# Kernel optimization log

Hardware: AMD Instinct MI355X
Metric: run time of the kernel (lower is better)

Reference implementation:

```python
import jax, jax.numpy as jnp
import numpy as np

N = 307
T = 6000
ED = 96
DIM_FC = 95712  # 16 * 5982
EPS_BN = 1e-5
TEMP = 0.5


def _conv1d(x, w, b):
    # x: [B, Cin, L], w: [Cout, Cin, K]
    y = jax.lax.conv_general_dilated(x, w, (1,), 'VALID',
                                     dimension_numbers=('NCH', 'OIH', 'NCH'))
    return y + b[None, :, None]


def _bn_nch(x, g, b):
    # BatchNorm1d on [B, C, L] in train mode (batch stats, biased var)
    m = jnp.mean(x, axis=(0, 2), keepdims=True)
    v = jnp.var(x, axis=(0, 2), keepdims=True)
    return g[None, :, None] * (x - m) * jax.lax.rsqrt(v + EPS_BN) + b[None, :, None]


def setup_inputs() -> dict:
    key = jax.random.key(0)
    ks = jax.random.split(key, 10)
    return {
        'long_term_history': jax.random.normal(ks[0], (32, 864, N), jnp.float32),
        'node_feats': jax.random.normal(ks[1], (T, N), jnp.float32),
        'conv1_w': jax.random.normal(ks[2], (8, 1, 10), jnp.float32) * 0.3,
        'conv1_b': jnp.zeros((8,), jnp.float32),
        'conv2_w': jax.random.normal(ks[3], (16, 8, 10), jnp.float32) * 0.1,
        'conv2_b': jnp.zeros((16,), jnp.float32),
        'bn1_g': jnp.ones((8,), jnp.float32),
        'bn1_b': jnp.zeros((8,), jnp.float32),
        'bn2_g': jnp.ones((16,), jnp.float32),
        'bn2_b': jnp.zeros((16,), jnp.float32),
        'bn3_g': jnp.ones((ED,), jnp.float32),
        'bn3_b': jnp.zeros((ED,), jnp.float32),
        'fc_w': jax.random.normal(ks[4], (DIM_FC, ED), jnp.float32) * 0.003,
        'fc_b': jnp.zeros((ED,), jnp.float32),
        'fc_out_w': jax.random.normal(ks[5], (2 * ED, ED), jnp.float32) * 0.07,
        'fc_out_b': jnp.zeros((ED,), jnp.float32),
        'fc_cat_w': jax.random.normal(ks[6], (ED, 2), jnp.float32) * 0.1,
        'fc_cat_b': jnp.zeros((2,), jnp.float32),
        'uniform': jax.random.uniform(ks[7], (N, N, 2), jnp.float32),
    }


def reference(long_term_history, node_feats, conv1_w, conv1_b, conv2_w, conv2_b,
              bn1_g, bn1_b, bn2_g, bn2_b, bn3_g, bn3_b, fc_w, fc_b,
              fc_out_w, fc_out_b, fc_cat_w, fc_cat_b, uniform):
    num_nodes = long_term_history.shape[2]
    # ---- node encoder (conv -> bn -> conv -> bn -> fc -> bn) ----
    x = node_feats.T[:, None, :]                              # [N, 1, T]
    x = _bn_nch(jax.nn.relu(_conv1d(x, conv1_w, conv1_b)), bn1_g, bn1_b)
    x = _bn_nch(jax.nn.relu(_conv1d(x, conv2_w, conv2_b)), bn2_g, bn2_b)
    x = x.reshape(num_nodes, -1)                              # [N, 95712]
    x = jax.nn.relu(x @ fc_w + fc_b)                          # [N, 96]
    m = jnp.mean(x, axis=0, keepdims=True)
    v = jnp.var(x, axis=0, keepdims=True)
    node_feat = bn3_g * (x - m) * jax.lax.rsqrt(v + EPS_BN) + bn3_b
    # ---- edge features: cat([sender, receiver]) @ W == s@Ws + r@Wr ----
    # edge e = i*N + j: sender = node_feat[j], receiver = node_feat[i]
    d = fc_out_w.shape[0] // 2
    s_proj = node_feat @ fc_out_w[:d]                         # [N, 96]
    r_proj = node_feat @ fc_out_w[d:]                         # [N, 96]
    edge_feat = jax.nn.relu(r_proj[:, None, :] + s_proj[None, :, :] + fc_out_b)  # [N, N, 96]
    logits = edge_feat @ fc_cat_w + fc_cat_b                  # [N, N, 2]
    # ---- hard gumbel-softmax ----
    gumbel = -jnp.log(-jnp.log(uniform + 1e-20) + 1e-20)
    y_soft = jax.nn.softmax((logits + gumbel) / TEMP, axis=-1)
    y_hard = jax.nn.one_hot(jnp.argmax(y_soft, axis=-1), 2, dtype=y_soft.dtype)
    y = jax.lax.stop_gradient(y_hard - y_soft) + y_soft
    adj = y[..., 0] * (1.0 - jnp.eye(num_nodes, dtype=y.dtype))  # zero diagonal
    return adj
```

## Files before the change

### kernel.cpp

```cpp
#include <hip/hip_runtime.h>
#include <hip/hip_fp16.h>

#define N_NODES 307
#define T_LEN   6000
#define L1      5991
#define L2      5982
#define ED      96
#define FDIM    95712
#define NCH2    16
#define LCPC    16
#define CHL     374
#define K5CH    (NCH2 * LCPC)
#define K3L     32
#define K3ZP    43
#define K3LB    187
#define K3NB    20
#define K3BLKS  (K3LB * K3NB)
#define K4ABLK  40
#define CSUB    8
#define CSROWS  47

static const size_t WS_P1 = 256;
static const size_t WS_P2 = 8192;
static const size_t WS_P4D = 127872;
static const size_t WS_NF = 155648;
static const size_t WS_SP = 188416;
static const size_t WS_RP = 221184;
static const size_t WS_A2 = 262144;
static const size_t WS_FP = 262144 + 30627840ull;
static const size_t WS_BP = 30889984ull + 7864320ull;
static const size_t WS_CS2 = 38754304ull + 9188352ull;

typedef _Float16 half8 __attribute__((ext_vector_type(8)));
typedef float f32x4 __attribute__((ext_vector_type(4)));

union U4H8 { uint4 u; half8 h; };

__device__ __forceinline__ unsigned int pack2h(float x) {
  __half h = __float2half(x);
  float r = (x - __half2float(h)) * 2048.0f;
  __half l = __float2half(r);
  return (unsigned int)__half_as_ushort(h) | ((unsigned int)__half_as_ushort(l) << 16);
}

__device__ __forceinline__ void split2h(float x, unsigned short& ho, unsigned short& lo) {
  __half h = __float2half(x);
  float r = (x - __half2float(h)) * 2048.0f;
  __half l = __float2half(r);
  ho = __half_as_ushort(h);
  lo = __half_as_ushort(l);
}

__device__ __forceinline__ void unpackU4(const uint4& a0, const uint4& a1,
                                         U4H8& hi, U4H8& lo) {
  hi.u = make_uint4((a0.x & 0xFFFFu) | (a0.y << 16), (a0.z & 0xFFFFu) | (a0.w << 16),
                    (a1.x & 0xFFFFu) | (a1.y << 16), (a1.z & 0xFFFFu) | (a1.w << 16));
  lo.u = make_uint4((a0.x >> 16) | (a0.y & 0xFFFF0000u), (a0.z >> 16) | (a0.w & 0xFFFF0000u),
                    (a1.x >> 16) | (a1.y & 0xFFFF0000u), (a1.z >> 16) | (a1.w & 0xFFFF0000u));
}

__device__ __forceinline__ int swz16(int e, int k) {
  return e * 192 + (k ^ ((e & 7) << 3));
}

__global__ __launch_bounds__(320) void dgl_k1_conv1_stats(
    const float* __restrict__ nfeat, const float* __restrict__ w1,
    const float* __restrict__ b1, float* __restrict__ ws) {
  __shared__ float sw1[80], sb1[8];
  __shared__ float sred[5][16];
  int tid = threadIdx.x;
  if (tid < 80) sw1[tid] = w1[tid];
  if (tid < 8)  sb1[tid] = b1[tid];
  __syncthreads();
  int l0 = blockIdx.x * 16;
  int n = tid;
  bool nv = n < N_NODES;
  float xx[26];
#pragma unroll
  for (int j = 0; j < 26; ++j) {
    int t = l0 + j;
    xx[j] = (nv && t < T_LEN) ? nfeat[(size_t)t * N_NODES + n] : 0.f;
  }
  float s[8], q[8];
#pragma unroll
  for (int c = 0; c < 8; ++c) { s[c] = 0.f; q[c] = 0.f; }
#pragma unroll
  for (int dl = 0; dl < 16; ++dl) {
    int l = l0 + dl;
    if (nv && l < L1) {
#pragma unroll
      for (int c = 0; c < 8; ++c) {
        float r = sb1[c];
#pragma unroll
        for (int k = 0; k < 10; ++k) r = fmaf(xx[dl + k], sw1[c * 10 + k], r);
        float z = fmaxf(r, 0.f);
        s[c] += z; q[c] += z * z;
      }
    }
  }
  int wv = tid >> 6, ln = tid & 63;
#pragma unroll
  for (int c = 0; c < 8; ++c) {
    float vs = s[c], vq = q[c];
    for (int o = 32; o; o >>= 1) { vs += __shfl_down(vs, o, 64); vq += __shfl_down(vq, o, 64); }
    if (ln == 0) { sred[wv][c] = vs; sred[wv][8 + c] = vq; }
  }
  __syncthreads();
  if (tid < 16) {
    float t = 0.f;
    for (int w = 0; w < 5; ++w) t += sred[w][tid];
    ws[WS_P1 + (size_t)blockIdx.x * 16 + tid] = t;
  }
}

__global__ void dgl_k2_fin1(const float* __restrict__ g1, const float* __restrict__ b1,
                            float* __restrict__ ws) {
  __shared__ double sd[16];
  int tid = threadIdx.x;
  if (tid < 16) {
    double a = 0.0;
    for (int j = 0; j < 375; ++j) a += (double)ws[WS_P1 + (size_t)j * 16 + tid];
    sd[tid] = a;
  }
  __syncthreads();
  if (tid < 8) {
    double cnt = (double)N_NODES * (double)L1;
    double m = sd[tid] / cnt;
    double v = sd[tid + 8] / cnt - m * m;
    double inv = 1.0 / sqrt(v + 1e-5);
    ws[tid]     = (float)((double)g1[tid] * inv);
    ws[8 + tid] = (float)((double)b1[tid] - (double)g1[tid] * inv * m);
  }
}

__global__ __launch_bounds__(256, 4) void dgl_k3_conv2(
    const float* __restrict__ nfeat, const float* __restrict__ w1, const float* __restrict__ b1,
    const float* __restrict__ w2, const float* __restrict__ b2, float* __restrict__ ws) {
  __shared__ __align__(16) unsigned short z1h[K3ZP * 128];
  __shared__ __align__(16) unsigned short z1l[K3ZP * 128];
  __shared__ __align__(16) unsigned short w2h[16 * 96], w2l[16 * 96];
  __shared__ float sw1[80], sb1[8], ss1[8], st1[8], sb2v[16];
  __shared__ float wps[4][4][4], wpq[4][4][4];
  int tid = threadIdx.x;
  int l0b = blockIdx.x * K3L, n0 = blockIdx.y * 16;
  unsigned int* a2u = (unsigned int*)(ws + WS_A2);

  if (tid < 80) sw1[tid] = w1[tid];
  if (tid < 8)  { sb1[tid] = b1[tid]; ss1[tid] = ws[tid]; st1[tid] = ws[8 + tid]; }
  if (tid < 16) sb2v[tid] = b2[tid];
  for (int i = tid; i < 16 * 96; i += 256) {
    int c2 = i / 96, kk = i % 96;
    float v = (kk < 80) ? w2[c2 * 80 + (kk & 7) * 10 + (kk >> 3)] : 0.f;
    unsigned short ho, lo;
    split2h(v, ho, lo);
    w2h[i] = ho; w2l[i] = lo;
  }
  __syncthreads();
  {
    int n = tid & 15, cin = (tid >> 4) & 7, hf = tid >> 7;
    int lp0 = hf ? 22 : 0;
    int cnt = hf ? 21 : 22;
    int nld = hf ? 30 : 31;
    int nglob0 = n0 + n;
    bool nv = nglob0 < N_NODES;
    float xx[31];
#pragma unroll
    for (int j = 0; j < 31; ++j) {
      int t = l0b + lp0 + j;
      xx[j] = (j < nld && nv && t < T_LEN) ? nfeat[(size_t)t * N_NODES + nglob0] : 0.f;
    }
    float wr[10];
#pragma unroll
    for (int k = 0; k < 10; ++k) wr[k] = sw1[cin * 10 + k];
    float bb = sb1[cin], sc = ss1[cin], sh = st1[cin];
#pragma unroll
    for (int o = 0; o < 22; ++o) {
      if (o < cnt) {
        float r = bb;
#pragma unroll
        for (int k = 0; k < 10; ++k) r = fmaf(xx[o + k], wr[k], r);
        float z = fmaf(sc, fmaxf(r, 0.f), sh);
        unsigned short ho, lo;
        split2h(z, ho, lo);
        int lp = lp0 + o;
        int idx = lp * 128 + ((n ^ (lp & 15)) << 3) + cin;
        z1h[idx] = ho; z1l[idx] = lo;
      }
    }
  }
  __syncthreads();

  int wv = tid >> 6, lane = tid & 63;
  int m = lane & 15, g = lane >> 4;
  U4H8 Ahi[3], Alo[3];
#pragma unroll
  for (int s = 0; s < 3; ++s) {
    Ahi[s].u = *(const uint4*)(&w2h[m * 96 + 32 * s + 8 * g]);
    Alo[s].u = *(const uint4*)(&w2l[m * 96 + 32 * s + 8 * g]);
  }
  float sv[4] = {0.f, 0.f, 0.f, 0.f}, qv[4] = {0.f, 0.f, 0.f, 0.f};
  int nglob = n0 + m;
  bool nok = nglob < N_NODES;
#pragma unroll 1
  for (int li = 0; li < 8; ++li) {
    int ll = 8 * wv + li;
    int lg = l0b + ll;
    f32x4 ac1 = (f32x4){0.f, 0.f, 0.f, 0.f};
    f32x4 ac2 = (f32x4){0.f, 0.f, 0.f, 0.f};
#pragma unroll
    for (int s = 0; s < 3; ++s) {
      int lp = ll + 4 * s + g;
      int bpidx = lp * 128 + ((m ^ (lp & 15)) << 3);
      U4H8 Bhi, Blo;
      Bhi.u = *(const uint4*)(&z1h[bpidx]);
      Blo.u = *(const uint4*)(&z1l[bpidx]);
      ac1 = __builtin_amdgcn_mfma_f32_16x16x32_f16(Ahi[s].h, Bhi.h, ac1, 0, 0, 0);
      ac2 = __builtin_amdgcn_mfma_f32_16x16x32_f16(Ahi[s].h, Blo.h, ac2, 0, 0, 0);
      ac2 = __builtin_amdgcn_mfma_f32_16x16x32_f16(Alo[s].h, Bhi.h, ac2, 0, 0, 0);
    }
    if (lg < L2) {
#pragma unroll
      for (int r = 0; r < 4; ++r) {
        float v = ac1[r] + ac2[r] * (1.0f / 2048.0f) + sb2v[4 * g + r];
        v = fmaxf(v, 0.f);
        if (!nok) v = 0.f;
        sv[r] += v; qv[r] += v * v;
        a2u[((size_t)(4 * g + r) * L2 + lg) * 320 + nglob] = pack2h(v);
      }
    }
  }
#pragma unroll
  for (int r = 0; r < 4; ++r) {
    for (int o = 1; o < 16; o <<= 1) {
      sv[r] += __shfl_xor(sv[r], o, 64);
      qv[r] += __shfl_xor(qv[r], o, 64);
    }
  }
  if (m == 0) {
#pragma unroll
    for (int r = 0; r < 4; ++r) { wps[wv][g][r] = sv[r]; wpq[wv][g][r] = qv[r]; }
  }
  __syncthreads();
  if (tid < 32) {
    int c2 = tid & 15; bool isq = tid >= 16;
    int gg = c2 >> 2, rr = c2 & 3;
    float t = 0.f;
    for (int w = 0; w < 4; ++w) t += isq ? wpq[w][gg][rr] : wps[w][gg][rr];
    ws[WS_P2 + ((size_t)blockIdx.y * gridDim.x + blockIdx.x) * 32 + tid] = t;
  }
}

__global__ __launch_bounds__(512) void dgl_k4a(float* __restrict__ ws) {
  __shared__ double red[16][32];
  int tid = threadIdx.x, blk = blockIdx.x;
  int v = tid & 31, p = tid >> 5;
  double a = 0.0;
#pragma unroll
  for (int k = 0; k < 6; ++k) {
    int idx = p + 16 * k;
    int j = blk * 94 + idx;
    if (idx < 94 && j < K3BLKS) a += (double)ws[WS_P2 + (size_t)j * 32 + v];
  }
  red[p][v] = a;
  __syncthreads();
  if (p == 0) {
    double s = 0.0;
    for (int q = 0; q < 16; ++q) s += red[q][v];
    ((double*)(ws + WS_P4D))[(size_t)blk * 32 + v] = s;
  }
}

__global__ void dgl_k4b2_fin(const float* __restrict__ g2, const float* __restrict__ b2,
                             float* __restrict__ ws) {
  __shared__ double sd[32];
  int tid = threadIdx.x;
  if (tid < 32) {
    const double* pd = (const double*)(ws + WS_P4D);
    double s = 0.0;
    for (int b = 0; b < K4ABLK; ++b) s += pd[(size_t)b * 32 + tid];
    sd[tid] = s;
  }
  __syncthreads();
  if (tid < 16) {
    double cnt = (double)N_NODES * (double)L2;
    double m = sd[tid] / cnt;
    double var = sd[tid + 16] / cnt - m * m;
    double inv = 1.0 / sqrt(var + 1e-5);
    ws[16 + tid] = (float)((double)g2[tid] * inv);
    ws[32 + tid] = (float)((double)b2[tid] - (double)g2[tid] * inv * m);
  }
}

__global__ __launch_bounds__(256) void dgl_k4b_colsum(const float* __restrict__ fcw,
                                                      float* __restrict__ ws) {
  __shared__ float red[10][96];
  int b = blockIdx.x;
  int ch = b >> 3, sub = b & 7;
  int lc = ch & (LCPC - 1);
  int clen = (lc == LCPC - 1) ? (L2 - CHL * (LCPC - 1)) : CHL;
  size_t fb = (size_t)(ch >> 4) * L2 + (size_t)lc * CHL;
  int r0 = sub * CSROWS;
  int r1 = min(clen, r0 + CSROWS);
  unsigned int* bpu = (unsigned int*)(ws + WS_BP);
  int tid = threadIdx.x;
  int e4 = tid % 24, rseg = tid / 24;
  if (rseg < 10) {
    float4 cs = make_float4(0.f, 0.f, 0.f, 0.f);
    for (int r = r0 + rseg; r < r1; r += 10) {
      float4 v = *(const float4*)(fcw + (fb + r) * 96 + e4 * 4);
      uint4 p;
      p.x = pack2h(v.x); p.y = pack2h(v.y); p.z = pack2h(v.z); p.w = pack2h(v.w);
      *(uint4*)(bpu + (fb + r) * 96 + e4 * 4) = p;
      cs.x += v.x; cs.y += v.y; cs.z += v.z; cs.w += v.w;
    }
    *(float4*)(&red[rseg][e4 * 4]) = cs;
  }
  __syncthreads();
  if (tid < 96) {
    float t = 0.f;
#pragma unroll
    for (int s = 0; s < 10; ++s) t += red[s][tid];
    ws[WS_CS2 + (size_t)b * 96 + tid] = t;
  }
}

__global__ __launch_bounds__(320, 2) void dgl_k5_fc(float* __restrict__ ws) {
  __shared__ __align__(16) unsigned short Bh[96 * 192];
  __shared__ __align__(16) unsigned short Bl[96 * 192];
  int tid = threadIdx.x;
  int ch = blockIdx.x;
  int nbase = blockIdx.y * 160;
  int lc = ch & (LCPC - 1);
  int clen = (lc == LCPC - 1) ? (L2 - CHL * (LCPC - 1)) : CHL;
  size_t fb = (size_t)(ch >> 4) * L2 + (size_t)lc * CHL;
  const unsigned int* a2u = (const unsigned int*)(ws + WS_A2);
  const unsigned int* bpu = (const unsigned int*)(ws + WS_BP);
  int wv = tid >> 6, lane = tid & 63;
  int m = lane & 15, g = lane >> 4;

  f32x4 acc1[2][6], acc2[2][6];
#pragma unroll
  for (int s = 0; s < 2; ++s)
#pragma unroll
    for (int t = 0; t < 6; ++t) {
      acc1[s][t] = (f32x4){0.f, 0.f, 0.f, 0.f};
      acc2[s][t] = (f32x4){0.f, 0.f, 0.f, 0.f};
    }

#pragma unroll 1
  for (int half = 0; half < 2; ++half) {
    int kb0 = half * 192;
#pragma unroll 1
    for (int it = 0; it < 15; ++it) {
      int idx = tid + it * 320;
      if (idx < 4608) {
        int r = idx % 192, eg = idx / 192;
        int rg = kb0 + r;
        uint4 v = (rg < clen) ? *(const uint4*)(bpu + (fb + rg) * 96 + eg * 4)
                              : make_uint4(0u, 0u, 0u, 0u);
        int e0 = eg * 4;
        Bh[swz16(e0 + 0, r)] = (unsigned short)(v.x & 0xFFFFu);
        Bl[swz16(e0 + 0, r)] = (unsigned short)(v.x >> 16);
        Bh[swz16(e0 + 1, r)] = (unsigned short)(v.y & 0xFFFFu);
        Bl[swz16(e0 + 1, r)] = (unsigned short)(v.y >> 16);
        Bh[swz16(e0 + 2, r)] = (unsigned short)(v.z & 0xFFFFu);
        Bl[swz16(e0 + 2, r)] = (unsigned short)(v.z >> 16);
        Bh[swz16(e0 + 3, r)] = (unsigned short)(v.w & 0xFFFFu);
        Bl[swz16(e0 + 3, r)] = (unsigned short)(v.w >> 16);
      }
    }
    __syncthreads();
#pragma unroll 1
    for (int ks = 0; ks < 6; ++ks) {
      int kbase = kb0 + ks * 32;
      int lim = clen - kbase;
      U4H8 Ahi[2], Alo[2];
#pragma unroll
      for (int s = 0; s < 2; ++s) {
        unsigned int au[8];
        int nt = wv + 5 * s;
        const unsigned int* abase =
            a2u + ((size_t)(fb + kbase + 8 * g)) * 320 + nbase + nt * 16 + m;
        if (lim >= 32) {
#pragma unroll
          for (int j = 0; j < 8; ++j) au[j] = abase[(size_t)j * 320];
        } else {
#pragma unroll
          for (int j = 0; j < 8; ++j) {
            int kk2 = 8 * g + j;
            au[j] = (kk2 < lim) ? abase[(size_t)j * 320] : 0u;
          }
        }
        uint4 a0 = make_uint4(au[0], au[1], au[2], au[3]);
        uint4 a1 = make_uint4(au[4], au[5], au[6], au[7]);
        unpackU4(a0, a1, Ahi[s], Alo[s]);
      }
#pragma unroll
      for (int t = 0; t < 6; ++t) {
        int e = 16 * t + m;
        int kl = ks * 32 + 8 * g;
        int kidx = swz16(e, kl);
        U4H8 Bhi, Blo;
        Bhi.u = *(const uint4*)(&Bh[kidx]);
        Blo.u = *(const uint4*)(&Bl[kidx]);
        acc1[0][t] = __builtin_amdgcn_mfma_f32_16x16x32_f16(Ahi[0].h, Bhi.h, acc1[0][t], 0, 0, 0);
        acc2[0][t] = __builtin_amdgcn_mfma_f32_16x16x32_f16(Ahi[0].h, Blo.h, acc2[0][t], 0, 0, 0);
        acc2[0][t] = __builtin_amdgcn_mfma_f32_16x16x32_f16(Alo[0].h, Bhi.h, acc2[0][t], 0, 0, 0);
        acc1[1][t] = __builtin_amdgcn_mfma_f32_16x16x32_f16(Ahi[1].h, Bhi.h, acc1[1][t], 0, 0, 0);
        acc2[1][t] = __builtin_amdgcn_mfma_f32_16x16x32_f16(Ahi[1].h, Blo.h, acc2[1][t], 0, 0, 0);
        acc2[1][t] = __builtin_amdgcn_mfma_f32_16x16x32_f16(Alo[1].h, Bhi.h, acc2[1][t], 0, 0, 0);
      }
    }
    __syncthreads();
  }
  float* fp = ws + WS_FP;
#pragma unroll
  for (int s = 0; s < 2; ++s) {
    int nt = wv + 5 * s;
#pragma unroll
    for (int t = 0; t < 6; ++t) {
      int e = 16 * t + m;
      float4 o;
      o.x = acc1[s][t][0] + acc2[s][t][0] * (1.0f / 2048.0f);
      o.y = acc1[s][t][1] + acc2[s][t][1] * (1.0f / 2048.0f);
      o.z = acc1[s][t][2] + acc2[s][t][2] * (1.0f / 2048.0f);
      o.w = acc1[s][t][3] + acc2[s][t][3] * (1.0f / 2048.0f);
      *(float4*)(fp + ((size_t)ch * 96 + e) * 320 + nbase + nt * 16 + 4 * g) = o;
    }
  }
}

__global__ __launch_bounds__(320) void dgl_k6a(float* __restrict__ ws) {
  int e = blockIdx.x, grp = blockIdx.y, n = threadIdx.x;
  const float* fp = ws + WS_FP;
  double* pd = (double*)(ws + WS_A2);
  double a = 0.0;
#pragma unroll
  for (int ci = 0; ci < 2; ++ci) {
    int c = grp * 2 + ci;
    double pc = 0.0;
#pragma unroll
    for (int lcv = 0; lcv < LCPC; ++lcv)
      pc += (double)fp[((size_t)(c * LCPC + lcv) * 96 + e) * 320 + n];
    a += (double)ws[16 + c] * pc;
  }
  pd[((size_t)e * 8 + grp) * 320 + n] = a;
}

__global__ __launch_bounds__(320) void dgl_k6b(const float* __restrict__ fcb,
                                               const float* __restrict__ g3,
                                               const float* __restrict__ b3,
                                               float* __restrict__ ws) {
  int e = blockIdx.x, tid = threadIdx.x;
  __shared__ double csd[16];
  __shared__ double rs[5], rq[5];
  __shared__ float mb[2];
  if (tid < 16) {
    double a = 0.0;
    for (int s = 0; s < LCPC * CSUB; ++s)
      a += (double)ws[WS_CS2 + (size_t)(tid * LCPC * CSUB + s) * 96 + e];
    csd[tid] = a * (double)ws[32 + tid];
  }
  __syncthreads();
  const double* pd = (const double*)(ws + WS_A2);
  double a = 0.0;
#pragma unroll
  for (int grp = 0; grp < 8; ++grp) a += pd[((size_t)e * 8 + grp) * 320 + tid];
  double cst = 0.0;
#pragma unroll
  for (int c = 0; c < 16; ++c) cst += csd[c];
  float x = fmaxf((float)(a + cst) + fcb[e], 0.f);
  if (tid >= N_NODES) x = 0.f;
  double s = (double)x, q = (double)x * (double)x;
  int wv = tid >> 6, ln = tid & 63;
  for (int o = 32; o; o >>= 1) { s += __shfl_down(s, o, 64); q += __shfl_down(q, o, 64); }
  if (ln == 0) { rs[wv] = s; rq[wv] = q; }
  __syncthreads();
  if (tid == 0) {
    double S = 0.0, Q = 0.0;
    for (int w = 0; w < 5; ++w) { S += rs[w]; Q += rq[w]; }
    double m = S / (double)N_NODES;
    double var = Q / (double)N_NODES - m * m;
    mb[0] = (float)m; mb[1] = (float)(1.0 / sqrt(var + 1e-5));
  }
  __syncthreads();
  if (tid < N_NODES)
    ws[WS_NF + (size_t)tid * 96 + e] = g3[e] * (x - mb[0]) * mb[1] + b3[e];
}

__global__ __launch_bounds__(192) void dgl_k7_proj(const float* __restrict__ fow,
                                                   float* __restrict__ ws) {
  __shared__ float sh[96];
  int nI = blockIdx.x, tid = threadIdx.x;
  if (tid < 96) sh[tid] = ws[WS_NF + (size_t)nI * 96 + tid];
  __syncthreads();
  int col = tid % 96, half = tid / 96;
  float a = 0.f;
#pragma unroll 8
  for (int d = 0; d < 96; ++d) a = fmaf(sh[d], fow[(size_t)(half * 96 + d) * 96 + col], a);
  ws[(half ? WS_RP : WS_SP) + (size_t)nI * 96 + col] = a;
}

__global__ __launch_bounds__(256) void dgl_k8_edge(const float* __restrict__ fob,
                                                   const float* __restrict__ fcatw,
                                                   const float* __restrict__ fcatb,
                                                   const float* __restrict__ unif,
                                                   const float* __restrict__ ws,
                                                   float* __restrict__ out) {
  __shared__ float rp[16][100], sp[16][100], bb[96], wa[96], wb[96];
  int tid = threadIdx.x;
  int i0 = blockIdx.y * 16, j0 = blockIdx.x * 16;
  for (int idx = tid; idx < 16 * 96; idx += 256) {
    int r = idx / 96, e = idx % 96;
    int ii = i0 + r, jj = j0 + r;
    rp[r][e] = (ii < N_NODES) ? ws[WS_RP + (size_t)ii * 96 + e] : 0.f;
    sp[r][e] = (jj < N_NODES) ? ws[WS_SP + (size_t)jj * 96 + e] : 0.f;
  }
  if (tid < 96) { bb[tid] = fob[tid]; wa[tid] = fcatw[2 * tid]; wb[tid] = fcatw[2 * tid + 1]; }
  __syncthreads();
  int il = tid >> 4, jl = tid & 15;
  int i = i0 + il, j = j0 + jl;
  float a0 = 0.f, a1 = 0.f;
#pragma unroll 4
  for (int e = 0; e < 96; ++e) {
    float ef = fmaxf(rp[il][e] + sp[jl][e] + bb[e], 0.f);
    a0 = fmaf(ef, wa[e], a0);
    a1 = fmaf(ef, wb[e], a1);
  }
  if (i < N_NODES && j < N_NODES) {
    size_t ue = ((size_t)i * N_NODES + j) * 2;
    float g0 = -logf(-logf(unif[ue] + 1e-20f) + 1e-20f);
    float g1 = -logf(-logf(unif[ue + 1] + 1e-20f) + 1e-20f);
    float z0 = a0 + fcatb[0] + g0;
    float z1 = a1 + fcatb[1] + g1;
    out[(size_t)i * N_NODES + j] = (i == j) ? 0.f : ((z0 >= z1) ? 1.f : 0.f);
  }
}

extern "C" void kernel_launch(void* const* d_in, const int* in_sizes, int n_in,
                              void* d_out, int out_size, void* d_ws, size_t ws_size,
                              hipStream_t stream) {
  const float* nfeat = (const float*)d_in[1];
  const float* w1    = (const float*)d_in[2];
  const float* b1    = (const float*)d_in[3];
  const float* w2    = (const float*)d_in[4];
  const float* b2    = (const float*)d_in[5];
  const float* g1    = (const float*)d_in[6];
  const float* bb1   = (const float*)d_in[7];
  const float* g2    = (const float*)d_in[8];
  const float* bb2   = (const float*)d_in[9];
  const float* g3    = (const float*)d_in[10];
  const float* bb3   = (const float*)d_in[11];
  const float* fcw   = (const float*)d_in[12];
  const float* fcb   = (const float*)d_in[13];
  const float* fow   = (const float*)d_in[14];
  const float* fob   = (const float*)d_in[15];
  const float* fcatw = (const float*)d_in[16];
  const float* fcatb = (const float*)d_in[17];
  const float* unif  = (const float*)d_in[18];
  float* ws  = (float*)d_ws;
  float* out = (float*)d_out;

  dgl_k4b_colsum<<<dim3(K5CH * CSUB), dim3(256), 0, stream>>>(fcw, ws);
  dgl_k1_conv1_stats<<<dim3(375), dim3(320), 0, stream>>>(nfeat, w1, b1, ws);
  dgl_k2_fin1<<<dim3(1), dim3(64), 0, stream>>>(g1, bb1, ws);
  dgl_k3_conv2<<<dim3(K3LB, K3NB), dim3(256), 0, stream>>>(nfeat, w1, b1, w2, b2, ws);
  dgl_k4a<<<dim3(K4ABLK), dim3(512), 0, stream>>>(ws);
  dgl_k4b2_fin<<<dim3(1), dim3(64), 0, stream>>>(g2, bb2, ws);
  dgl_k5_fc<<<dim3(K5CH, 2), dim3(320), 0, stream>>>(ws);
  dgl_k6a<<<dim3(96, 8), dim3(320), 0, stream>>>(ws);
  dgl_k6b<<<dim3(96), dim3(320), 0, stream>>>(fcb, g3, bb3, ws);
  dgl_k7_proj<<<dim3(307), dim3(192), 0, stream>>>(fow, ws);
  dgl_k8_edge<<<dim3(20, 20), dim3(256), 0, stream>>>(fob, fcatw, fcatb, unif, ws, out);
}
```

Measured before the change: 180.3 us.

## Store conv2 activations in k-grouped blocked layout for vectorized FC loads

Conv2 output is re-laid out so that each node's eight consecutive L positions for a channel sit together in one 32-byte group. The conv2 kernel buffers eight results in registers and writes them as two uint4 stores, and the FC kernel reads its A fragments with two vector loads instead of eight strided scalar loads with bounds checks. The tail group is zero-padded, so the per-chunk length becomes 376 and a small zeroing kernel is added. The cost is an extra launch, more workspace, and extra registers in conv2.

```diff
diff --git a/kernel.cpp b/kernel.cpp
--- a/kernel.cpp
+++ b/kernel.cpp
@@ -9,7 +9,8 @@
 #define FDIM    95712
 #define NCH2    16
 #define LCPC    16
-#define CHL     374
+#define CHL     376
+#define NGRP    753
 #define K5CH    (NCH2 * LCPC)
 #define K3L     32
 #define K3ZP    43
@@ -27,9 +28,9 @@
 static const size_t WS_SP = 188416;
 static const size_t WS_RP = 221184;
 static const size_t WS_A2 = 262144;
-static const size_t WS_FP = 262144 + 30627840ull;
-static const size_t WS_BP = 30889984ull + 7864320ull;
-static const size_t WS_CS2 = 38754304ull + 9188352ull;
+static const size_t WS_FP = 262144 + 30842880ull;
+static const size_t WS_BP = 31105024ull + 7864320ull;
+static const size_t WS_CS2 = 38969344ull + 9188352ull;
 
 typedef _Float16 half8 __attribute__((ext_vector_type(8)));
 typedef float f32x4 __attribute__((ext_vector_type(4)));
@@ -61,6 +62,14 @@
 
 __device__ __forceinline__ int swz16(int e, int k) {
   return e * 192 + (k ^ ((e & 7) << 3));
+}
+
+__global__ __launch_bounds__(256) void dgl_k0_zero(float* __restrict__ ws) {
+  unsigned int* a2k = (unsigned int*)(ws + WS_A2);
+  int idx = blockIdx.x * 256 + threadIdx.x;
+  int c = idx / 3840, off4 = idx % 3840;
+  unsigned int* p = a2k + (((size_t)c * NGRP + 747) * 320) * 8 + (size_t)off4 * 4;
+  *(uint4*)p = make_uint4(0u, 0u, 0u, 0u);
 }
 
 __global__ __launch_bounds__(320) void dgl_k1_conv1_stats(
@@ -143,7 +152,7 @@
   __shared__ float wps[4][4][4], wpq[4][4][4];
   int tid = threadIdx.x;
   int l0b = blockIdx.x * K3L, n0 = blockIdx.y * 16;
-  unsigned int* a2u = (unsigned int*)(ws + WS_A2);
+  unsigned int* a2k = (unsigned int*)(ws + WS_A2);
 
   if (tid < 80) sw1[tid] = w1[tid];
   if (tid < 8)  { sb1[tid] = b1[tid]; ss1[tid] = ws[tid]; st1[tid] = ws[8 + tid]; }
@@ -199,6 +208,7 @@
     Alo[s].u = *(const uint4*)(&w2l[m * 96 + 32 * s + 8 * g]);
   }
   float sv[4] = {0.f, 0.f, 0.f, 0.f}, qv[4] = {0.f, 0.f, 0.f, 0.f};
+  unsigned int outw[4][8];
   int nglob = n0 + m;
   bool nok = nglob < N_NODES;
 #pragma unroll 1
@@ -218,15 +228,23 @@
       ac2 = __builtin_amdgcn_mfma_f32_16x16x32_f16(Ahi[s].h, Blo.h, ac2, 0, 0, 0);
       ac2 = __builtin_amdgcn_mfma_f32_16x16x32_f16(Alo[s].h, Bhi.h, ac2, 0, 0, 0);
     }
-    if (lg < L2) {
-#pragma unroll
-      for (int r = 0; r < 4; ++r) {
-        float v = ac1[r] + ac2[r] * (1.0f / 2048.0f) + sb2v[4 * g + r];
-        v = fmaxf(v, 0.f);
-        if (!nok) v = 0.f;
-        sv[r] += v; qv[r] += v * v;
-        a2u[((size_t)(4 * g + r) * L2 + lg) * 320 + nglob] = pack2h(v);
-      }
+#pragma unroll
+    for (int r = 0; r < 4; ++r) {
+      float v = ac1[r] + ac2[r] * (1.0f / 2048.0f) + sb2v[4 * g + r];
+      v = fmaxf(v, 0.f);
+      if (!nok || lg >= L2) v = 0.f;
+      sv[r] += v; qv[r] += v * v;
+      outw[r][li] = pack2h(v);
+    }
+  }
+  {
+    int grp = (l0b + 8 * wv) >> 3;
+#pragma unroll
+    for (int r = 0; r < 4; ++r) {
+      int c2 = 4 * g + r;
+      unsigned int* p = a2k + (((size_t)c2 * NGRP + grp) * 320 + nglob) * 8;
+      *(uint4*)p = make_uint4(outw[r][0], outw[r][1], outw[r][2], outw[r][3]);
+      *(uint4*)(p + 4) = make_uint4(outw[r][4], outw[r][5], outw[r][6], outw[r][7]);
     }
   }
 #pragma unroll
@@ -330,13 +348,14 @@
   int tid = threadIdx.x;
   int ch = blockIdx.x;
   int nbase = blockIdx.y * 160;
-  int lc = ch & (LCPC - 1);
+  int c = ch >> 4, lc = ch & (LCPC - 1);
   int clen = (lc == LCPC - 1) ? (L2 - CHL * (LCPC - 1)) : CHL;
-  size_t fb = (size_t)(ch >> 4) * L2 + (size_t)lc * CHL;
-  const unsigned int* a2u = (const unsigned int*)(ws + WS_A2);
+  size_t fb = (size_t)c * L2 + (size_t)lc * CHL;
+  const unsigned int* a2k = (const unsigned int*)(ws + WS_A2);
   const unsigned int* bpu = (const unsigned int*)(ws + WS_BP);
   int wv = tid >> 6, lane = tid & 63;
   int m = lane & 15, g = lane >> 4;
+  int lc47 = lc * 47;
 
   f32x4 acc1[2][6], acc2[2][6];
 #pragma unroll
@@ -373,26 +392,15 @@
 #pragma unroll 1
     for (int ks = 0; ks < 6; ++ks) {
       int kbase = kb0 + ks * 32;
-      int lim = clen - kbase;
+      int grp0 = lc47 + (kbase >> 3) + g;
       U4H8 Ahi[2], Alo[2];
 #pragma unroll
       for (int s = 0; s < 2; ++s) {
-        unsigned int au[8];
         int nt = wv + 5 * s;
-        const unsigned int* abase =
-            a2u + ((size_t)(fb + kbase + 8 * g)) * 320 + nbase + nt * 16 + m;
-        if (lim >= 32) {
-#pragma unroll
-          for (int j = 0; j < 8; ++j) au[j] = abase[(size_t)j * 320];
-        } else {
-#pragma unroll
-          for (int j = 0; j < 8; ++j) {
-            int kk2 = 8 * g + j;
-            au[j] = (kk2 < lim) ? abase[(size_t)j * 320] : 0u;
-          }
-        }
-        uint4 a0 = make_uint4(au[0], au[1], au[2], au[3]);
-        uint4 a1 = make_uint4(au[4], au[5], au[6], au[7]);
+        int n = nbase + nt * 16 + m;
+        const unsigned int* ap = a2k + (((size_t)c * NGRP + grp0) * 320 + n) * 8;
+        uint4 a0 = *(const uint4*)ap;
+        uint4 a1 = *(const uint4*)(ap + 4);
         unpackU4(a0, a1, Ahi[s], Alo[s]);
       }
 #pragma unroll
@@ -561,6 +569,7 @@
   float* ws  = (float*)d_ws;
   float* out = (float*)d_out;
 
+  dgl_k0_zero<<<dim3(240), dim3(256), 0, stream>>>(ws);
   dgl_k4b_colsum<<<dim3(K5CH * CSUB), dim3(256), 0, stream>>>(fcw, ws);
   dgl_k1_conv1_stats<<<dim3(375), dim3(320), 0, stream>>>(nfeat, w1, b1, ws);
   dgl_k2_fin1<<<dim3(1), dim3(64), 0, stream>>>(g1, bb1, ws);
```

After: 188.1 us. +4.3%, slower.
